# Optimization experiments

Hardware: AMD Instinct MI355X
Metric: run time of the kernel (lower is better)

The kernel has to match this reference:

```python
import jax, jax.numpy as jnp
import numpy as np

B, N, DIM, H, DH = 4, 2048, 1024, 16, 64
ROT = 32               # rotary dim (half of head dim)
INNER = H * DH         # 1024


def rotate_every_two(x):
    # (... (d j)) with j=2: pairs (x1, x2) -> (-x2, x1), interleaved back
    x1 = x[..., ::2]
    x2 = x[..., 1::2]
    return jnp.stack((-x2, x1), axis=-1).reshape(x.shape)


def setup_inputs() -> dict:
    key = jax.random.key(0)
    k1, k2, k3 = jax.random.split(key, 3)
    x = jax.random.normal(k1, (B, N, DIM), dtype=jnp.float32)
    # standard rotary sin/cos tables, [N, ROT], pairs share a frequency
    pos = jnp.arange(N, dtype=jnp.float32)[:, None]
    inv_freq = 1.0 / (10000.0 ** (jnp.arange(0, ROT, 2, dtype=jnp.float32) / ROT))
    ang = jnp.repeat(pos * inv_freq, 2, axis=-1)  # [N, ROT]
    sin, cos = jnp.sin(ang), jnp.cos(ang)
    Wqkv = jax.random.normal(k2, (DIM, 3 * INNER), dtype=jnp.float32) * (DIM ** -0.5)
    Wout = jax.random.normal(k3, (INNER, DIM), dtype=jnp.float32) * (INNER ** -0.5)
    return {"x": x, "sin": sin, "cos": cos, "Wqkv": Wqkv, "Wout": Wout}


def reference(x, sin, cos, Wqkv, Wout):
    scale = DH ** -0.5
    qkv = x @ Wqkv                                  # [B, N, 3*INNER]
    q, k, v = jnp.split(qkv, 3, axis=-1)

    def split_heads(t):  # 'b n (h d) -> (b h) n d'
        return t.reshape(B, N, H, DH).transpose(0, 2, 1, 3).reshape(B * H, N, DH)

    q, k, v = map(split_heads, (q, k, v))
    q = q * scale                                   # scale before RoPE (as in source)

    rd = sin.shape[-1]

    def rope(t):
        t_rot, t_pass = t[..., :rd], t[..., rd:]
        t_rot = t_rot * cos + rotate_every_two(t_rot) * sin
        return jnp.concatenate((t_rot, t_pass), axis=-1)

    q, k = rope(q), rope(k)

    sim = jnp.einsum('bid,bjd->bij', q, k)          # [(B*H), N, N]
    attn_w = jax.nn.softmax(sim, axis=-1)
    out = jnp.einsum('bij,bjd->bid', attn_w, v)     # [(B*H), N, DH]

    out = out.reshape(B, H, N, DH).transpose(0, 2, 1, 3).reshape(B, N, INNER)
    return out @ Wout                               # [B, N, DIM]
```

## Files before the change

kernel.cpp:

```cpp
#include <hip/hip_runtime.h>

typedef unsigned short u16;
typedef __attribute__((ext_vector_type(8))) short short8;
typedef __attribute__((ext_vector_type(4))) float f32x4;

#define DEV __device__ __forceinline__

DEV u16 f2bf(float f) {
  unsigned u = __float_as_uint(f);
  u += 0x7FFF + ((u >> 16) & 1);
  return (u16)(u >> 16);
}
DEV float bf2f(u16 b) { return __uint_as_float(((unsigned)b) << 16); }

DEV unsigned pk_trunc(float a, float b) {
  return __builtin_amdgcn_perm(__float_as_uint(b), __float_as_uint(a), 0x07060302u);
}

DEV void g2l16(const u16* g, u16* l) {
  __builtin_amdgcn_global_load_lds((__attribute__((address_space(1))) void*)(g),
                                   (__attribute__((address_space(3))) void*)(l), 16, 0, 0);
}

__global__ __launch_bounds__(256) void k_prep(const float* __restrict__ x,
                                              u16* __restrict__ xb,
                                              const float* __restrict__ Wqkv,
                                              u16* __restrict__ wqkvT,
                                              const float* __restrict__ Wout,
                                              u16* __restrict__ woutT) {
  __shared__ float t[32][33];
  const int blk = blockIdx.x;
  if (blk < 8192) {
    int i = blk * 256 + threadIdx.x;
    float4 v = ((const float4*)x)[i];
    ushort4 r;
    r.x = f2bf(v.x); r.y = f2bf(v.y); r.z = f2bf(v.z); r.w = f2bf(v.w);
    ((ushort4*)xb)[i] = r;
    return;
  }
  const float* W;
  u16* Wt;
  int K = 1024, N, local;
  if (blk < 11264) {
    W = Wqkv; Wt = wqkvT; N = 3072; local = blk - 8192;
  } else {
    W = Wout; Wt = woutT; N = 1024; local = blk - 11264;
  }
  int nb = N / 32;
  int n0 = (local % nb) * 32, k0 = (local / nb) * 32;
  int tx = threadIdx.x & 31, ty = threadIdx.x >> 5;
#pragma unroll
  for (int i = 0; i < 4; ++i)
    t[ty + i * 8][tx] = W[(size_t)(k0 + ty + i * 8) * N + n0 + tx];
  __syncthreads();
#pragma unroll
  for (int i = 0; i < 4; ++i)
    Wt[(size_t)(n0 + ty + i * 8) * K + k0 + tx] = f2bf(t[tx][ty + i * 8]);
}

__global__ __launch_bounds__(512, 2) void k_gemm0(
    const u16* __restrict__ A, const u16* __restrict__ Bt,
    u16* __restrict__ qw, u16* __restrict__ kw, u16* __restrict__ vw,
    const float* __restrict__ sn, const float* __restrict__ cs, float qscale) {
  __shared__ __align__(16) u16 As[2][2][8192];
  __shared__ __align__(16) u16 Bs[2][2][8192];
  const int tid = threadIdx.x;
  const int wid = tid >> 6, lane = tid & 63;
  const int a15 = lane & 15, g = lane >> 4;
  const int wr = wid >> 2, wc = wid & 3;
  const int m0 = (blockIdx.x & 31) * 256, n0 = (blockIdx.x >> 5) * 256;
  const int K = 1024;
  const int srow = wid * 8 + (lane >> 3);
  const int scol = ((lane & 7) ^ (lane >> 3)) << 3;
  const int swz = (a15 & 7) << 4;

#define SA(s, h, l, u) g2l16(A + (size_t)(m0 + (h)*128 + (l)*64 + srow) * K + (u)*64 + scol, \
                             &As[s][h][(l)*4096 + wid * 512])
#define SB(s, h, l, u) g2l16(Bt + (size_t)(n0 + (h)*128 + (l)*64 + srow) * K + (u)*64 + scol, \
                             &Bs[s][h][(l)*4096 + wid * 512])

  f32x4 acc[8][4];
#pragma unroll
  for (int i = 0; i < 8; ++i)
#pragma unroll
    for (int j = 0; j < 4; ++j)
#pragma unroll
      for (int r = 0; r < 4; ++r) acc[i][j][r] = 0.f;

  SA(0,0,0,0); SA(0,1,0,0); SA(0,0,1,0); SA(0,1,1,0);
  SB(0,0,0,0); SB(0,0,1,0); SB(0,1,0,0); SB(0,1,1,0);
  SA(1,0,0,1); SA(1,1,0,1); SA(1,0,1,1); SA(1,1,1,1);
  SB(1,0,0,1); SB(1,0,1,1); SB(1,1,0,1); SB(1,1,1,1);
  asm volatile("s_waitcnt vmcnt(8)" ::: "memory");
  __builtin_amdgcn_s_barrier();

  short8 af[4][2], bf[4][2];
  const int brb = (wc & 1) * 64;

  for (int t = 0; t < 16; ++t) {
    const int s = t & 1, u = t + 2;
    const bool st = (u < 16);
    const char* Ab = (const char*)&As[s][wr][0];
    const char* Bb = (const char*)&Bs[s][wc >> 1][0];
#pragma unroll
    for (int mi = 0; mi < 4; ++mi)
#pragma unroll
      for (int ks = 0; ks < 2; ++ks)
        af[mi][ks] = *(const short8*)(Ab + (((mi * 16 + a15) * 128 + ks * 64 + g * 16) ^ swz));
#pragma unroll
    for (int ni = 0; ni < 2; ++ni)
#pragma unroll
      for (int ks = 0; ks < 2; ++ks)
        bf[ni][ks] = *(const short8*)(Bb + (((brb + ni * 16 + a15) * 128 + ks * 64 + g * 16) ^ swz));
    __builtin_amdgcn_s_barrier();
    __builtin_amdgcn_s_setprio(1);
#pragma unroll
    for (int mi = 0; mi < 4; ++mi)
#pragma unroll
      for (int ni = 0; ni < 2; ++ni)
#pragma unroll
        for (int ks = 0; ks < 2; ++ks)
          acc[mi][ni] = __builtin_amdgcn_mfma_f32_16x16x32_bf16(af[mi][ks], bf[ni][ks], acc[mi][ni], 0, 0, 0);
    __builtin_amdgcn_s_setprio(0);
    __builtin_amdgcn_s_barrier();
    if (st) { SA(s, 0, 0, u); SA(s, 1, 0, u); }
#pragma unroll
    for (int ni = 0; ni < 2; ++ni)
#pragma unroll
      for (int ks = 0; ks < 2; ++ks)
        bf[2 + ni][ks] = *(const short8*)(Bb + (((brb + (2 + ni) * 16 + a15) * 128 + ks * 64 + g * 16) ^ swz));
    __builtin_amdgcn_s_barrier();
    __builtin_amdgcn_s_setprio(1);
#pragma unroll
    for (int mi = 0; mi < 4; ++mi)
#pragma unroll
      for (int ni = 0; ni < 2; ++ni)
#pragma unroll
        for (int ks = 0; ks < 2; ++ks)
          acc[mi][2 + ni] = __builtin_amdgcn_mfma_f32_16x16x32_bf16(af[mi][ks], bf[2 + ni][ks], acc[mi][2 + ni], 0, 0, 0);
    __builtin_amdgcn_s_setprio(0);
    __builtin_amdgcn_s_barrier();
    if (st) { SB(s, 0, 0, u); SB(s, 0, 1, u); }
#pragma unroll
    for (int mi = 0; mi < 4; ++mi)
#pragma unroll
      for (int ks = 0; ks < 2; ++ks)
        af[mi][ks] = *(const short8*)(Ab + ((((64 + mi * 16) + a15) * 128 + ks * 64 + g * 16) ^ swz));
    __builtin_amdgcn_s_barrier();
    __builtin_amdgcn_s_setprio(1);
#pragma unroll
    for (int mi = 0; mi < 4; ++mi)
#pragma unroll
      for (int ni = 0; ni < 2; ++ni)
#pragma unroll
        for (int ks = 0; ks < 2; ++ks)
          acc[4 + mi][ni] = __builtin_amdgcn_mfma_f32_16x16x32_bf16(af[mi][ks], bf[ni][ks], acc[4 + mi][ni], 0, 0, 0);
    __builtin_amdgcn_s_setprio(0);
    __builtin_amdgcn_s_barrier();
    if (st) { SA(s, 0, 1, u); SA(s, 1, 1, u); }
    __builtin_amdgcn_s_barrier();
    __builtin_amdgcn_s_setprio(1);
#pragma unroll
    for (int mi = 0; mi < 4; ++mi)
#pragma unroll
      for (int ni = 0; ni < 2; ++ni)
#pragma unroll
        for (int ks = 0; ks < 2; ++ks)
          acc[4 + mi][2 + ni] = __builtin_amdgcn_mfma_f32_16x16x32_bf16(af[mi][ks], bf[2 + ni][ks], acc[4 + mi][2 + ni], 0, 0, 0);
    __builtin_amdgcn_s_setprio(0);
    if (st) { SB(s, 1, 0, u); SB(s, 1, 1, u); }
    if (t < 14) {
      asm volatile("s_waitcnt vmcnt(8)" ::: "memory");
    } else if (t == 14) {
      asm volatile("s_waitcnt vmcnt(0)" ::: "memory");
    }
    __builtin_amdgcn_s_barrier();
  }
#undef SA
#undef SB

  const int part = n0 >> 10;
  if (part <= 1) {
    const float sc = (part == 0) ? qscale : 1.f;
    u16* dst = (part == 0) ? qw : kw;
#pragma unroll
    for (int mi = 0; mi < 8; ++mi) {
#pragma unroll
      for (int ni = 0; ni < 4; ++ni) {
        int col = n0 + wc * 64 + ni * 16 + a15;
        int rem = col & 1023, h = rem >> 6, d = rem & 63;
        int row = m0 + wr * 128 + mi * 16 + g * 4;
        int b = row >> 11, n = row & 2047;
        size_t bh = (size_t)b * 16 + h;
#pragma unroll
        for (int r = 0; r < 4; ++r) {
          float v = acc[mi][ni][r];
          float p = __shfl_xor(v, 1);
          float outv = v;
          if (d < 32) {
            int nr = n + r;
            float c = cs[nr * 32 + d], s2 = sn[nr * 32 + d];
            outv = v * c + ((d & 1) ? p * s2 : -p * s2);
          }
          dst[(bh * 2048 + n + r) * 64 + d] = f2bf(outv * sc);
        }
      }
    }
  } else {
#pragma unroll
    for (int mi = 0; mi < 8; ++mi) {
#pragma unroll
      for (int ni = 0; ni < 4; ++ni) {
        int col = n0 + wc * 64 + ni * 16 + a15;
        int rem = col & 1023, h = rem >> 6, d = rem & 63;
        int row = m0 + wr * 128 + mi * 16 + g * 4;
        int b = row >> 11, n = row & 2047;
        size_t bh = (size_t)b * 16 + h;
        ushort4 pk;
        pk.x = f2bf(acc[mi][ni][0]); pk.y = f2bf(acc[mi][ni][1]);
        pk.z = f2bf(acc[mi][ni][2]); pk.w = f2bf(acc[mi][ni][3]);
        *(ushort4*)&vw[(bh * 64 + d) * 2048 + n] = pk;
      }
    }
  }
}

template <int EPI>
__global__ __launch_bounds__(256) void k_gemm(
    const u16* __restrict__ A, const u16* __restrict__ Bt,
    int M, int N, int K, float* __restrict__ of) {
  __shared__ __align__(16) u16 As[128 * 64];
  __shared__ __align__(16) u16 Bs[128 * 64];
  const int t = threadIdx.x;
  const int wv = t >> 6, lane = t & 63;
  const int a15 = lane & 15, g = lane >> 4;
  const int wr = wv >> 1, wc = wv & 1;
  const int m0 = blockIdx.x * 128, n0 = blockIdx.y * 128;
  const int gr = lane >> 3, gc = (lane & 7) * 8;

  f32x4 acc[4][4];
#pragma unroll
  for (int i = 0; i < 4; ++i)
#pragma unroll
    for (int j = 0; j < 4; ++j)
#pragma unroll
      for (int r = 0; r < 4; ++r) acc[i][j][r] = 0.f;

  for (int k0 = 0; k0 < K; k0 += 64) {
#pragma unroll
    for (int c4 = 0; c4 < 4; ++c4) {
      int c = wv * 4 + c4;
      g2l16(A + (size_t)(m0 + c * 8 + gr) * K + k0 + gc, &As[c * 512]);
      g2l16(Bt + (size_t)(n0 + c * 8 + gr) * K + k0 + gc, &Bs[c * 512]);
    }
    __syncthreads();
#pragma unroll
    for (int ks = 0; ks < 2; ++ks) {
      short8 af[4], bf[4];
#pragma unroll
      for (int mi = 0; mi < 4; ++mi)
        af[mi] = *(const short8*)&As[(wr * 64 + mi * 16 + a15) * 64 + ks * 32 + g * 8];
#pragma unroll
      for (int ni = 0; ni < 4; ++ni)
        bf[ni] = *(const short8*)&Bs[(wc * 64 + ni * 16 + a15) * 64 + ks * 32 + g * 8];
#pragma unroll
      for (int mi = 0; mi < 4; ++mi)
#pragma unroll
        for (int ni = 0; ni < 4; ++ni)
          acc[mi][ni] = __builtin_amdgcn_mfma_f32_16x16x32_bf16(af[mi], bf[ni], acc[mi][ni], 0, 0, 0);
    }
    __syncthreads();
  }

#pragma unroll
  for (int mi = 0; mi < 4; ++mi)
#pragma unroll
    for (int ni = 0; ni < 4; ++ni) {
      int col = n0 + wc * 64 + ni * 16 + a15;
      int row = m0 + wr * 64 + mi * 16 + g * 4;
#pragma unroll
      for (int r = 0; r < 4; ++r)
        of[(size_t)(row + r) * N + col] = acc[mi][ni][r];
    }
}

__global__ __launch_bounds__(256, 3) void k_attn(
    const u16* __restrict__ q, const u16* __restrict__ kk, const u16* __restrict__ vT,
    u16* __restrict__ o) {
  __shared__ __align__(16) u16 Ks[2][4096];
  __shared__ __align__(16) u16 Vs[2][4096];
  __shared__ __align__(16) u16 Pl[4][1024];
  const int t = threadIdx.x;
  const int w = t >> 6, lane = t & 63;
  const int a15 = lane & 15, g = lane >> 4;
  const int id = blockIdx.x;
  const int bh = (id & 7) | ((id >> 7) << 3);
  const int qb = (id >> 3) & 15;
  const int q0 = qb * 128 + w * 32;
  const size_t hb = (size_t)bh * (2048 * 64);

  short8 qf[2][2];
#pragma unroll
  for (int f = 0; f < 2; ++f)
#pragma unroll
    for (int h = 0; h < 2; ++h)
      qf[f][h] = *(const short8*)&q[hb + (size_t)(q0 + f * 16 + a15) * 64 + h * 32 + g * 8];

  int ksrc[2], vsrc[2];
#pragma unroll
  for (int c = 0; c < 2; ++c) {
    int L = w * 2048 + c * 1024 + lane * 16;
    int row = L >> 7;
    int sb = L ^ ((row & 7) << 4);
    ksrc[c] = sb >> 1;
    vsrc[c] = row * 2048 + ((sb & 127) >> 1);
  }
  const u16* kg = kk + hb;
  const u16* vg = vT + (size_t)bh * (64 * 2048);

#define STAGE(b, j0) do {                                        \
    g2l16(kg + (size_t)(j0) * 64 + ksrc[0], &Ks[b][w * 1024]);   \
    g2l16(kg + (size_t)(j0) * 64 + ksrc[1], &Ks[b][w * 1024 + 512]); \
    g2l16(vg + (j0) + vsrc[0], &Vs[b][w * 1024]);                \
    g2l16(vg + (j0) + vsrc[1], &Vs[b][w * 1024 + 512]);          \
  } while (0)

  const f32x4 z4 = {0.f, 0.f, 0.f, 0.f};
  const short8 ones = {(short)0x3F80, (short)0x3F80, (short)0x3F80, (short)0x3F80,
                       (short)0x3F80, (short)0x3F80, (short)0x3F80, (short)0x3F80};
  f32x4 accO[2][4], ssum[2];
#pragma unroll
  for (int f = 0; f < 2; ++f) {
    ssum[f] = z4;
#pragma unroll
    for (int dc = 0; dc < 4; ++dc) accO[f][dc] = z4;
  }

  STAGE(0, 0);
  int cur = 0;
  for (int jt = 0; jt < 32; ++jt) {
    __syncthreads();
    if (jt < 31) STAGE(cur ^ 1, (jt + 1) * 64);

    f32x4 st[2][4];
    const char* Kb = (const char*)Ks[cur];
    __builtin_amdgcn_s_setprio(1);
#pragma unroll
    for (int jc = 0; jc < 4; ++jc) {
      int row = jc * 16 + a15;
      int sw = (row & 7) << 4;
      short8 ka0 = *(const short8*)(Kb + ((row * 128 + g * 16) ^ sw));
      short8 ka1 = *(const short8*)(Kb + ((row * 128 + 64 + g * 16) ^ sw));
      st[0][jc] = __builtin_amdgcn_mfma_f32_16x16x32_bf16(ka0, qf[0][0], z4, 0, 0, 0);
      st[0][jc] = __builtin_amdgcn_mfma_f32_16x16x32_bf16(ka1, qf[0][1], st[0][jc], 0, 0, 0);
      st[1][jc] = __builtin_amdgcn_mfma_f32_16x16x32_bf16(ka0, qf[1][0], z4, 0, 0, 0);
      st[1][jc] = __builtin_amdgcn_mfma_f32_16x16x32_bf16(ka1, qf[1][1], st[1][jc], 0, 0, 0);
    }
    __builtin_amdgcn_s_setprio(0);
    short8 vf[2][4];
    const char* Vb = (const char*)Vs[cur];
#pragma unroll
    for (int kt = 0; kt < 2; ++kt)
#pragma unroll
      for (int dc = 0; dc < 4; ++dc) {
        int row = dc * 16 + a15;
        vf[kt][dc] = *(const short8*)(Vb + ((row * 128 + kt * 64 + g * 16) ^ ((row & 7) << 4)));
      }
#pragma unroll
    for (int f = 0; f < 2; ++f) {
#pragma unroll
      for (int jc = 0; jc < 4; ++jc) {
        float e0 = __builtin_amdgcn_exp2f(st[f][jc][0]);
        float e1 = __builtin_amdgcn_exp2f(st[f][jc][1]);
        float e2 = __builtin_amdgcn_exp2f(st[f][jc][2]);
        float e3 = __builtin_amdgcn_exp2f(st[f][jc][3]);
        uint2 pw;
        pw.x = pk_trunc(e0, e1);
        pw.y = pk_trunc(e2, e3);
        int byte = (a15 * 128 + (jc * 16 + g * 4) * 2) ^ ((a15 & 7) << 4);
        *(uint2*)((char*)Pl[w] + byte) = pw;
      }
      __builtin_amdgcn_s_setprio(1);
#pragma unroll
      for (int kt = 0; kt < 2; ++kt) {
        int byteA = (a15 * 128 + kt * 64 + g * 16) ^ ((a15 & 7) << 4);
        short8 pa = *(const short8*)((const char*)Pl[w] + byteA);
        ssum[f] = __builtin_amdgcn_mfma_f32_16x16x32_bf16(pa, ones, ssum[f], 0, 0, 0);
#pragma unroll
        for (int dc = 0; dc < 4; ++dc)
          accO[f][dc] = __builtin_amdgcn_mfma_f32_16x16x32_bf16(pa, vf[kt][dc], accO[f][dc], 0, 0, 0);
      }
      __builtin_amdgcn_s_setprio(0);
    }
    cur ^= 1;
  }
#undef STAGE

  const int b = bh >> 4, h = bh & 15;
#pragma unroll
  for (int f = 0; f < 2; ++f) {
    float rs[4];
#pragma unroll
    for (int r = 0; r < 4; ++r) rs[r] = 1.f / ssum[f][r];
#pragma unroll
    for (int dc = 0; dc < 4; ++dc)
#pragma unroll
      for (int r = 0; r < 4; ++r) {
        int n = q0 + f * 16 + g * 4 + r;
        o[((size_t)b * 2048 + n) * 1024 + h * 64 + dc * 16 + a15] = f2bf(accO[f][dc][r] * rs[r]);
      }
  }
}

extern "C" void kernel_launch(void* const* d_in, const int* in_sizes, int n_in,
                              void* d_out, int out_size, void* d_ws, size_t ws_size,
                              hipStream_t stream) {
  const float* x = (const float*)d_in[0];
  const float* sn = (const float*)d_in[1];
  const float* cs = (const float*)d_in[2];
  const float* Wqkv = (const float*)d_in[3];
  const float* Wout = (const float*)d_in[4];
  float* out = (float*)d_out;

  u16* ws = (u16*)d_ws;
  u16* xb = ws;
  u16* wqkvT = xb + 8192ull * 1024;
  u16* woutT = wqkvT + 3072ull * 1024;
  u16* qw = woutT + 1024ull * 1024;
  u16* kw = qw + 64ull * 2048 * 64;
  u16* vw = kw + 64ull * 2048 * 64;
  u16* attn = xb;

  const float qscale = 0.125f * 1.4426950408889634f;

  k_prep<<<12288, 256, 0, stream>>>(x, xb, Wqkv, wqkvT, Wout, woutT);
  k_gemm0<<<384, 512, 0, stream>>>(xb, wqkvT, qw, kw, vw, sn, cs, qscale);
  k_attn<<<1024, 256, 0, stream>>>(qw, kw, vw, attn);
  k_gemm<1><<<dim3(64, 8), 256, 0, stream>>>(attn, woutT, 8192, 1024, 1024, out);
}
```

Before: 213.5 us.

## Reshape QKV GEMM tiles to 256x192 for 512 blocks

Changes the QKV projection GEMM tile from 256x256 to 256x192, raising the grid from 384 to 512 blocks. Each wave now covers 48 output columns (three 16-wide MFMA column tiles) instead of 64. The LDS staging, load schedule and vmcnt waits are reworked to match, and the epilogue now picks q/k/v per column because a tile can straddle a part boundary. The goal is better balance across the CUs (512 blocks vs 384) at the cost of less data reuse per tile and a per-column branch in the epilogue.

```diff
diff --git a/kernel.cpp b/kernel.cpp
--- a/kernel.cpp
+++ b/kernel.cpp
@@ -62,56 +62,53 @@
     const u16* __restrict__ A, const u16* __restrict__ Bt,
     u16* __restrict__ qw, u16* __restrict__ kw, u16* __restrict__ vw,
     const float* __restrict__ sn, const float* __restrict__ cs, float qscale) {
-  __shared__ __align__(16) u16 As[2][2][8192];
-  __shared__ __align__(16) u16 Bs[2][2][8192];
+  __shared__ __align__(16) u16 As[2][16384];
+  __shared__ __align__(16) u16 Bs[2][12288];
   const int tid = threadIdx.x;
   const int wid = tid >> 6, lane = tid & 63;
   const int a15 = lane & 15, g = lane >> 4;
   const int wr = wid >> 2, wc = wid & 3;
-  const int m0 = (blockIdx.x & 31) * 256, n0 = (blockIdx.x >> 5) * 256;
+  const int m0 = (blockIdx.x & 31) * 256, n0 = (blockIdx.x >> 5) * 192;
   const int K = 1024;
   const int srow = wid * 8 + (lane >> 3);
   const int scol = ((lane & 7) ^ (lane >> 3)) << 3;
   const int swz = (a15 & 7) << 4;
 
-#define SA(s, h, l, u) g2l16(A + (size_t)(m0 + (h)*128 + (l)*64 + srow) * K + (u)*64 + scol, \
-                             &As[s][h][(l)*4096 + wid * 512])
-#define SB(s, h, l, u) g2l16(Bt + (size_t)(n0 + (h)*128 + (l)*64 + srow) * K + (u)*64 + scol, \
-                             &Bs[s][h][(l)*4096 + wid * 512])
-
-  f32x4 acc[8][4];
+#define SA(s, c, u) g2l16(A + (size_t)(m0 + (c)*64 + srow) * K + (u)*64 + scol, \
+                          &As[s][(c)*4096 + wid * 512])
+#define SB(s, c, u) g2l16(Bt + (size_t)(n0 + (c)*64 + srow) * K + (u)*64 + scol, \
+                          &Bs[s][(c)*4096 + wid * 512])
+
+  f32x4 acc[8][3];
 #pragma unroll
   for (int i = 0; i < 8; ++i)
 #pragma unroll
-    for (int j = 0; j < 4; ++j)
+    for (int j = 0; j < 3; ++j)
 #pragma unroll
       for (int r = 0; r < 4; ++r) acc[i][j][r] = 0.f;
 
-  SA(0,0,0,0); SA(0,1,0,0); SA(0,0,1,0); SA(0,1,1,0);
-  SB(0,0,0,0); SB(0,0,1,0); SB(0,1,0,0); SB(0,1,1,0);
-  SA(1,0,0,1); SA(1,1,0,1); SA(1,0,1,1); SA(1,1,1,1);
-  SB(1,0,0,1); SB(1,0,1,1); SB(1,1,0,1); SB(1,1,1,1);
-  asm volatile("s_waitcnt vmcnt(8)" ::: "memory");
+  SA(0,0,0); SA(0,1,0); SA(0,2,0); SA(0,3,0); SB(0,0,0); SB(0,1,0); SB(0,2,0);
+  SA(1,0,1); SA(1,1,1); SA(1,2,1); SA(1,3,1); SB(1,0,1); SB(1,1,1); SB(1,2,1);
+  asm volatile("s_waitcnt vmcnt(7)" ::: "memory");
   __builtin_amdgcn_s_barrier();
 
-  short8 af[4][2], bf[4][2];
-  const int brb = (wc & 1) * 64;
+  short8 af[4][2], bf[3][2];
 
   for (int t = 0; t < 16; ++t) {
     const int s = t & 1, u = t + 2;
     const bool st = (u < 16);
-    const char* Ab = (const char*)&As[s][wr][0];
-    const char* Bb = (const char*)&Bs[s][wc >> 1][0];
+    const char* Ab = (const char*)&As[s][0];
+    const char* Bb = (const char*)&Bs[s][0];
 #pragma unroll
     for (int mi = 0; mi < 4; ++mi)
 #pragma unroll
       for (int ks = 0; ks < 2; ++ks)
-        af[mi][ks] = *(const short8*)(Ab + (((mi * 16 + a15) * 128 + ks * 64 + g * 16) ^ swz));
+        af[mi][ks] = *(const short8*)(Ab + (((wr * 128 + mi * 16 + a15) * 128 + ks * 64 + g * 16) ^ swz));
 #pragma unroll
     for (int ni = 0; ni < 2; ++ni)
 #pragma unroll
       for (int ks = 0; ks < 2; ++ks)
-        bf[ni][ks] = *(const short8*)(Bb + (((brb + ni * 16 + a15) * 128 + ks * 64 + g * 16) ^ swz));
+        bf[ni][ks] = *(const short8*)(Bb + (((wc * 48 + ni * 16 + a15) * 128 + ks * 64 + g * 16) ^ swz));
     __builtin_amdgcn_s_barrier();
     __builtin_amdgcn_s_setprio(1);
 #pragma unroll
@@ -123,29 +120,25 @@
           acc[mi][ni] = __builtin_amdgcn_mfma_f32_16x16x32_bf16(af[mi][ks], bf[ni][ks], acc[mi][ni], 0, 0, 0);
     __builtin_amdgcn_s_setprio(0);
     __builtin_amdgcn_s_barrier();
-    if (st) { SA(s, 0, 0, u); SA(s, 1, 0, u); }
-#pragma unroll
-    for (int ni = 0; ni < 2; ++ni)
+    if (st) { SA(s, 0, u); SA(s, 2, u); }
+#pragma unroll
+    for (int ks = 0; ks < 2; ++ks)
+      bf[2][ks] = *(const short8*)(Bb + (((wc * 48 + 32 + a15) * 128 + ks * 64 + g * 16) ^ swz));
+    __builtin_amdgcn_s_barrier();
+    __builtin_amdgcn_s_setprio(1);
+#pragma unroll
+    for (int mi = 0; mi < 4; ++mi)
 #pragma unroll
       for (int ks = 0; ks < 2; ++ks)
-        bf[2 + ni][ks] = *(const short8*)(Bb + (((brb + (2 + ni) * 16 + a15) * 128 + ks * 64 + g * 16) ^ swz));
-    __builtin_amdgcn_s_barrier();
-    __builtin_amdgcn_s_setprio(1);
-#pragma unroll
-    for (int mi = 0; mi < 4; ++mi)
-#pragma unroll
-      for (int ni = 0; ni < 2; ++ni)
-#pragma unroll
-        for (int ks = 0; ks < 2; ++ks)
-          acc[mi][2 + ni] = __builtin_amdgcn_mfma_f32_16x16x32_bf16(af[mi][ks], bf[2 + ni][ks], acc[mi][2 + ni], 0, 0, 0);
+        acc[mi][2] = __builtin_amdgcn_mfma_f32_16x16x32_bf16(af[mi][ks], bf[2][ks], acc[mi][2], 0, 0, 0);
     __builtin_amdgcn_s_setprio(0);
     __builtin_amdgcn_s_barrier();
-    if (st) { SB(s, 0, 0, u); SB(s, 0, 1, u); }
+    if (st) { SB(s, 0, u); SB(s, 1, u); }
 #pragma unroll
     for (int mi = 0; mi < 4; ++mi)
 #pragma unroll
       for (int ks = 0; ks < 2; ++ks)
-        af[mi][ks] = *(const short8*)(Ab + ((((64 + mi * 16) + a15) * 128 + ks * 64 + g * 16) ^ swz));
+        af[mi][ks] = *(const short8*)(Ab + (((wr * 128 + 64 + mi * 16 + a15) * 128 + ks * 64 + g * 16) ^ swz));
     __builtin_amdgcn_s_barrier();
     __builtin_amdgcn_s_setprio(1);
 #pragma unroll
@@ -157,20 +150,17 @@
           acc[4 + mi][ni] = __builtin_amdgcn_mfma_f32_16x16x32_bf16(af[mi][ks], bf[ni][ks], acc[4 + mi][ni], 0, 0, 0);
     __builtin_amdgcn_s_setprio(0);
     __builtin_amdgcn_s_barrier();
-    if (st) { SA(s, 0, 1, u); SA(s, 1, 1, u); }
+    if (st) { SA(s, 1, u); SA(s, 3, u); SB(s, 2, u); }
     __builtin_amdgcn_s_barrier();
     __builtin_amdgcn_s_setprio(1);
 #pragma unroll
     for (int mi = 0; mi < 4; ++mi)
 #pragma unroll
-      for (int ni = 0; ni < 2; ++ni)
-#pragma unroll
-        for (int ks = 0; ks < 2; ++ks)
-          acc[4 + mi][2 + ni] = __builtin_amdgcn_mfma_f32_16x16x32_bf16(af[mi][ks], bf[2 + ni][ks], acc[4 + mi][2 + ni], 0, 0, 0);
+      for (int ks = 0; ks < 2; ++ks)
+        acc[4 + mi][2] = __builtin_amdgcn_mfma_f32_16x16x32_bf16(af[mi][ks], bf[2][ks], acc[4 + mi][2], 0, 0, 0);
     __builtin_amdgcn_s_setprio(0);
-    if (st) { SB(s, 1, 0, u); SB(s, 1, 1, u); }
     if (t < 14) {
-      asm volatile("s_waitcnt vmcnt(8)" ::: "memory");
+      asm volatile("s_waitcnt vmcnt(7)" ::: "memory");
     } else if (t == 14) {
       asm volatile("s_waitcnt vmcnt(0)" ::: "memory");
     }
@@ -179,19 +169,19 @@
 #undef SA
 #undef SB
 
-  const int part = n0 >> 10;
-  if (part <= 1) {
-    const float sc = (part == 0) ? qscale : 1.f;
-    u16* dst = (part == 0) ? qw : kw;
-#pragma unroll
-    for (int mi = 0; mi < 8; ++mi) {
-#pragma unroll
-      for (int ni = 0; ni < 4; ++ni) {
-        int col = n0 + wc * 64 + ni * 16 + a15;
-        int rem = col & 1023, h = rem >> 6, d = rem & 63;
-        int row = m0 + wr * 128 + mi * 16 + g * 4;
-        int b = row >> 11, n = row & 2047;
-        size_t bh = (size_t)b * 16 + h;
+#pragma unroll
+  for (int mi = 0; mi < 8; ++mi) {
+    int row = m0 + wr * 128 + mi * 16 + g * 4;
+    int b = row >> 11, n = row & 2047;
+#pragma unroll
+    for (int ni = 0; ni < 3; ++ni) {
+      int col = n0 + wc * 48 + ni * 16 + a15;
+      int part = col >> 10;
+      int rem = col & 1023, h = rem >> 6, d = rem & 63;
+      size_t bh = (size_t)b * 16 + h;
+      if (part <= 1) {
+        const float sc = (part == 0) ? qscale : 1.f;
+        u16* dst = (part == 0) ? qw : kw;
 #pragma unroll
         for (int r = 0; r < 4; ++r) {
           float v = acc[mi][ni][r];
@@ -204,18 +194,7 @@
           }
           dst[(bh * 2048 + n + r) * 64 + d] = f2bf(outv * sc);
         }
-      }
-    }
-  } else {
-#pragma unroll
-    for (int mi = 0; mi < 8; ++mi) {
-#pragma unroll
-      for (int ni = 0; ni < 4; ++ni) {
-        int col = n0 + wc * 64 + ni * 16 + a15;
-        int rem = col & 1023, h = rem >> 6, d = rem & 63;
-        int row = m0 + wr * 128 + mi * 16 + g * 4;
-        int b = row >> 11, n = row & 2047;
-        size_t bh = (size_t)b * 16 + h;
+      } else {
         ushort4 pk;
         pk.x = f2bf(acc[mi][ni][0]); pk.y = f2bf(acc[mi][ni][1]);
         pk.z = f2bf(acc[mi][ni][2]); pk.w = f2bf(acc[mi][ni][3]);
@@ -434,7 +413,7 @@
   const float qscale = 0.125f * 1.4426950408889634f;
 
   k_prep<<<12288, 256, 0, stream>>>(x, xb, Wqkv, wqkvT, Wout, woutT);
-  k_gemm0<<<384, 512, 0, stream>>>(xb, wqkvT, qw, kw, vw, sn, cs, qscale);
+  k_gemm0<<<512, 512, 0, stream>>>(xb, wqkvT, qw, kw, vw, sn, cs, qscale);
   k_attn<<<1024, 256, 0, stream>>>(qw, kw, vw, attn);
   k_gemm<1><<<dim3(64, 8), 256, 0, stream>>>(attn, woutT, 8192, 1024, 1024, out);
 }
```

New measurement: 225.7 us. 5.7% more time.
